# Kernel tuning notes

Hardware: AMD Instinct MI355X
Metric: run time of the kernel (lower is better)

The kernel has to match this reference:

```python
import jax, jax.numpy as jnp
import numpy as np

NUM_LAYERS = 2
SHAPES = [(100, 100), (50, 50), (25, 25), (13, 13)]  # (H, W) per level
D, NH, NP, NL = 256, 8, 4, 4
DH = D // NH
DFF = 1024
B = 2
S = sum(h * w for h, w in SHAPES)  # 13294


def layer_norm(x, g, b, eps=1e-5):
    m = x.mean(-1, keepdims=True)
    v = jnp.var(x, axis=-1, keepdims=True)
    return (x - m) * jax.lax.rsqrt(v + eps) * g + b


def get_reference_points(valid_ratios):
    refs = []
    for lvl, (H_, W_) in enumerate(SHAPES):
        ry, rx = jnp.meshgrid(jnp.linspace(0.5, H_ - 0.5, H_),
                              jnp.linspace(0.5, W_ - 0.5, W_), indexing='ij')
        ry = ry.reshape(-1)[None] / (valid_ratios[:, None, lvl, 1] * H_)
        rx = rx.reshape(-1)[None] / (valid_ratios[:, None, lvl, 0] * W_)
        refs.append(jnp.stack([rx, ry], -1))
    ref = jnp.concatenate(refs, 1)                      # [B, S, 2]
    return ref[:, :, None] * valid_ratios[:, None]      # [B, S, NL, 2]


def sample_level(value_l, H_, W_, loc):
    # value_l: [B, nH, H*W, Dh]; loc: [B, Q, nH, P, 2] normalized in [0,1]
    x = loc[..., 0] * W_ - 0.5
    y = loc[..., 1] * H_ - 0.5
    x0 = jnp.floor(x)
    y0 = jnp.floor(y)
    Bq, Q = loc.shape[0], loc.shape[1]
    acc = 0.
    corners = ((x0, y0, (x0 + 1 - x) * (y0 + 1 - y)),
               (x0 + 1, y0, (x - x0) * (y0 + 1 - y)),
               (x0, y0 + 1, (x0 + 1 - x) * (y - y0)),
               (x0 + 1, y0 + 1, (x - x0) * (y - y0)))
    for xi, yi, w in corners:  # zero-padding grid_sample: invalid corners contribute 0
        valid = (xi >= 0) & (xi <= W_ - 1) & (yi >= 0) & (yi <= H_ - 1)
        idx = (jnp.clip(yi, 0, H_ - 1) * W_ + jnp.clip(xi, 0, W_ - 1)).astype(jnp.int32)
        idx = jnp.transpose(idx, (0, 2, 1, 3)).reshape(Bq, NH, Q * NP)
        g = jnp.take_along_axis(value_l, idx[..., None], axis=2)  # [B,nH,Q*P,Dh]
        wv = jnp.transpose((w * valid).astype(value_l.dtype), (0, 2, 1, 3)).reshape(Bq, NH, Q * NP)
        acc = acc + g * wv[..., None]
    return acc.reshape(Bq, NH, Q, NP, DH)


def msda(query, ref, src, W_val, b_val, W_off, b_off, W_attn, b_attn, W_out, b_out):
    Bq, Q = query.shape[:2]
    value = (src @ W_val + b_val).reshape(Bq, S, NH, DH)
    off = (query @ W_off + b_off).reshape(Bq, Q, NH, NL, NP, 2)
    attn = jax.nn.softmax((query @ W_attn + b_attn).reshape(Bq, Q, NH, NL * NP), -1)
    attn = attn.reshape(Bq, Q, NH, NL, NP)
    normalizer = jnp.array([[w, h] for h, w in SHAPES], dtype=query.dtype)  # [NL,2] (x,y)
    loc = ref[:, :, None, :, None, :] + off / normalizer[None, None, None, :, None, :]
    out = jnp.zeros((Bq, NH, Q, DH), query.dtype)
    start = 0
    for l, (H_, W_) in enumerate(SHAPES):
        v_l = jnp.transpose(value[:, start:start + H_ * W_], (0, 2, 1, 3))  # [B,nH,HW,Dh]
        samp = sample_level(v_l, H_, W_, loc[:, :, :, l])                    # [B,nH,Q,P,Dh]
        w_l = jnp.transpose(attn[:, :, :, l], (0, 2, 1, 3))                  # [B,nH,Q,P]
        out = out + (samp * w_l[..., None]).sum(3)
        start += H_ * W_
    out = jnp.transpose(out, (0, 2, 1, 3)).reshape(Bq, Q, D)
    return out @ W_out + b_out


def setup_inputs() -> dict:
    key = jax.random.key(0)
    ks = jax.random.split(key, 12)
    sc = 0.02
    inp = {
        'src': jax.random.normal(ks[0], (B, S, D), jnp.float32),
        'spatial_shapes': np.array(SHAPES, dtype=np.int64),
        'valid_ratios': jnp.ones((B, NL, 2), jnp.float32),
        'W_off': sc * jax.random.normal(ks[1], (NUM_LAYERS, D, NH * NL * NP * 2), jnp.float32),
        'b_off': jnp.zeros((NUM_LAYERS, NH * NL * NP * 2), jnp.float32),
        'W_attn': sc * jax.random.normal(ks[2], (NUM_LAYERS, D, NH * NL * NP), jnp.float32),
        'b_attn': jnp.zeros((NUM_LAYERS, NH * NL * NP), jnp.float32),
        'W_val': sc * jax.random.normal(ks[3], (NUM_LAYERS, D, D), jnp.float32),
        'b_val': jnp.zeros((NUM_LAYERS, D), jnp.float32),
        'W_out': sc * jax.random.normal(ks[4], (NUM_LAYERS, D, D), jnp.float32),
        'b_out': jnp.zeros((NUM_LAYERS, D), jnp.float32),
        'ln1_g': jnp.ones((NUM_LAYERS, D), jnp.float32),
        'ln1_b': jnp.zeros((NUM_LAYERS, D), jnp.float32),
        'W1': sc * jax.random.normal(ks[5], (NUM_LAYERS, D, DFF), jnp.float32),
        'b1': jnp.zeros((NUM_LAYERS, DFF), jnp.float32),
        'W2': sc * jax.random.normal(ks[6], (NUM_LAYERS, DFF, D), jnp.float32),
        'b2': jnp.zeros((NUM_LAYERS, D), jnp.float32),
        'ln2_g': jnp.ones((NUM_LAYERS, D), jnp.float32),
        'ln2_b': jnp.zeros((NUM_LAYERS, D), jnp.float32),
    }
    return inp


def reference(src, spatial_shapes, valid_ratios, W_off, b_off, W_attn, b_attn,
              W_val, b_val, W_out, b_out, ln1_g, ln1_b, W1, b1, W2, b2, ln2_g, ln2_b):
    # Deformable-DETR encoder stack (dropout=0 / eval mode, pos=None, no padding mask).
    ref = get_reference_points(valid_ratios)  # [B, S, NL, 2]
    x = src
    for i in range(NUM_LAYERS):
        x2 = msda(x, ref, x, W_val[i], b_val[i], W_off[i], b_off[i],
                  W_attn[i], b_attn[i], W_out[i], b_out[i])
        x = layer_norm(x + x2, ln1_g[i], ln1_b[i])
        h = jax.nn.relu(x @ W1[i] + b1[i]) @ W2[i] + b2[i]
        x = layer_norm(x + h, ln2_g[i], ln2_b[i])
    return x
```

## Files before the change

kernel.cpp:

```cpp
#include <hip/hip_runtime.h>
#include <math.h>


#define S_TOT 13294
#define BATCH 2
#define M_TOT (BATCH * S_TOT)
#define M_PAD 26624

typedef __attribute__((ext_vector_type(8))) short short8;
typedef __attribute__((ext_vector_type(4))) float floatx4;

#define AS1C(p) ((const __attribute__((address_space(1))) void*)(p))
#define AS3(p)  ((__attribute__((address_space(3))) void*)(p))

static __device__ __forceinline__ unsigned short f2bf(float x) {
    union { float f; unsigned u; } v; v.f = x;
    unsigned r = v.u + 0x7FFFu + ((v.u >> 16) & 1u);
    return (unsigned short)(r >> 16);
}
static __device__ __forceinline__ float bflo(unsigned u) {
    union { unsigned u; float f; } v; v.u = u << 16; return v.f;
}
static __device__ __forceinline__ float bfhi(unsigned u) {
    union { unsigned u; float f; } v; v.u = u & 0xFFFF0000u; return v.f;
}

template<int TM, bool RELU, bool RES, bool F32OUT, bool BF16OUT, bool PROJ>
__global__ __launch_bounds__(256)
void mgemm(const unsigned short* __restrict__ A,
           const unsigned short* __restrict__ BT,
           const float* __restrict__ bias,
           const float* __restrict__ bias2,
           const float* __restrict__ bias3,
           const float* __restrict__ R,
           float* __restrict__ Cf,
           unsigned short* __restrict__ Cb,
           int M, int N, int K)
{
    constexpr int WM = (TM == 128) ? 2 : 1;
    constexpr int WN = 4 / WM;
    constexpr int MI = TM / (WM * 16);
    constexpr int NI = 128 / (WN * 16);
    __shared__ __align__(16) unsigned short smemA[2 * TM * 32];
    __shared__ __align__(16) unsigned short smemB[2 * 128 * 32];
    const int tid  = threadIdx.x;
    const int lane = tid & 63;
    const int w    = tid >> 6;
    const int wm   = w % WM, wn = w / WM;
    const int lr   = lane & 15, quad = lane >> 4;
    const int bm   = blockIdx.y * TM;
    const int bn   = blockIdx.x * 128;

    floatx4 acc[MI][NI];
    #pragma unroll
    for (int i = 0; i < MI; ++i)
        #pragma unroll
        for (int j = 0; j < NI; ++j)
            acc[i][j] = (floatx4){0.f, 0.f, 0.f, 0.f};

    const int srow = lane >> 2;
    const int selt = (lane & 3) << 3;

    for (int k0 = 0; k0 < K; k0 += 64) {
        #pragma unroll
        for (int c = 0; c < 2; ++c) {
            if (TM == 128) {
                #pragma unroll
                for (int jj = 0; jj < 2; ++jj) {
                    const int j = 2 * w + jj;
                    const unsigned short* ga = A  + (size_t)(bm + j * 16 + srow) * K + k0 + c * 32 + selt;
                    const unsigned short* gb = BT + (size_t)(bn + j * 16 + srow) * K + k0 + c * 32 + selt;
                    __builtin_amdgcn_global_load_lds(AS1C(ga), AS3(smemA + c * (TM * 32) + j * 512), 16, 0, 0);
                    __builtin_amdgcn_global_load_lds(AS1C(gb), AS3(smemB + c * 4096 + j * 512), 16, 0, 0);
                }
            } else {
                const unsigned short* ga = A + (size_t)(bm + w * 16 + srow) * K + k0 + c * 32 + selt;
                __builtin_amdgcn_global_load_lds(AS1C(ga), AS3(smemA + c * (TM * 32) + w * 512), 16, 0, 0);
                #pragma unroll
                for (int jj = 0; jj < 2; ++jj) {
                    const int j = 2 * w + jj;
                    const unsigned short* gb = BT + (size_t)(bn + j * 16 + srow) * K + k0 + c * 32 + selt;
                    __builtin_amdgcn_global_load_lds(AS1C(gb), AS3(smemB + c * 4096 + j * 512), 16, 0, 0);
                }
            }
        }
        __syncthreads();

        #pragma unroll
        for (int c = 0; c < 2; ++c) {
            short8 av[MI], bv[NI];
            #pragma unroll
            for (int mi = 0; mi < MI; ++mi)
                av[mi] = *(const short8*)&smemA[c * (TM * 32) + (wm * MI * 16 + mi * 16 + lr) * 32 + quad * 8];
            #pragma unroll
            for (int ni = 0; ni < NI; ++ni)
                bv[ni] = *(const short8*)&smemB[c * 4096 + (wn * NI * 16 + ni * 16 + lr) * 32 + quad * 8];
            #pragma unroll
            for (int mi = 0; mi < MI; ++mi)
                #pragma unroll
                for (int ni = 0; ni < NI; ++ni)
                    acc[mi][ni] = __builtin_amdgcn_mfma_f32_16x16x32_bf16(
                        av[mi], bv[ni], acc[mi][ni], 0, 0, 0);
        }
        __syncthreads();
    }

    #pragma unroll
    for (int mi = 0; mi < MI; ++mi) {
        #pragma unroll
        for (int ni = 0; ni < NI; ++ni) {
            #pragma unroll
            for (int r = 0; r < 4; ++r) {
                const int row = bm + wm * MI * 16 + mi * 16 + quad * 4 + r;
                const int col = bn + wn * NI * 16 + ni * 16 + lr;
                if (PROJ) {
                    const float bb = (col < 256) ? bias[col]
                                   : (col < 512) ? bias2[col - 256]
                                                 : bias3[col - 512];
                    const float v = acc[mi][ni][r] + bb;
                    if (col < 256) Cb[(size_t)row * 256 + col] = f2bf(v);
                    else           Cf[(size_t)row * 384 + (col - 256)] = v;
                } else {
                    float v = acc[mi][ni][r] + bias[col];
                    if (RES) { if (row < M) v += R[(size_t)row * N + col]; }
                    if (RELU) v = fmaxf(v, 0.0f);
                    if (F32OUT) Cf[(size_t)row * N + col] = v;
                    if (BF16OUT) Cb[(size_t)row * N + col] = f2bf(v);
                }
            }
        }
    }
}

template<bool HASB>
__global__ __launch_bounds__(256)
void mgemm_ln(const unsigned short* __restrict__ A,
              const unsigned short* __restrict__ BT,
              const float* __restrict__ bias,
              const float* __restrict__ R,
              const float* __restrict__ g,
              const float* __restrict__ beta,
              float* __restrict__ outF,
              unsigned short* __restrict__ outB,
              int M, int K)
{
    __shared__ __align__(16) unsigned short smemA[2 * 64 * 32];
    __shared__ __align__(16) unsigned short smemB[2 * 256 * 32];
    const int lane = threadIdx.x & 63;
    const int w    = threadIdx.x >> 6;
    const int lr   = lane & 15, quad = lane >> 4;
    const int bm   = blockIdx.x * 64;
    const int srow = lane >> 2;
    const int selt = (lane & 3) << 3;

    floatx4 acc[4][4];
    #pragma unroll
    for (int i = 0; i < 4; ++i)
        #pragma unroll
        for (int j = 0; j < 4; ++j)
            acc[i][j] = (floatx4){0.f, 0.f, 0.f, 0.f};

    for (int k0 = 0; k0 < K; k0 += 64) {
        #pragma unroll
        for (int c = 0; c < 2; ++c) {
            const unsigned short* ga = A + (size_t)(bm + w * 16 + srow) * K + k0 + c * 32 + selt;
            __builtin_amdgcn_global_load_lds(AS1C(ga), AS3(smemA + c * 2048 + w * 512), 16, 0, 0);
            #pragma unroll
            for (int jj = 0; jj < 4; ++jj) {
                const int j = 4 * w + jj;
                const unsigned short* gb = BT + (size_t)(j * 16 + srow) * K + k0 + c * 32 + selt;
                __builtin_amdgcn_global_load_lds(AS1C(gb), AS3(smemB + c * 8192 + j * 512), 16, 0, 0);
            }
        }
        __syncthreads();
        #pragma unroll
        for (int c = 0; c < 2; ++c) {
            short8 av[4], bv[4];
            #pragma unroll
            for (int mi = 0; mi < 4; ++mi)
                av[mi] = *(const short8*)&smemA[c * 2048 + (mi * 16 + lr) * 32 + quad * 8];
            #pragma unroll
            for (int ni = 0; ni < 4; ++ni)
                bv[ni] = *(const short8*)&smemB[c * 8192 + (w * 64 + ni * 16 + lr) * 32 + quad * 8];
            #pragma unroll
            for (int mi = 0; mi < 4; ++mi)
                #pragma unroll
                for (int ni = 0; ni < 4; ++ni)
                    acc[mi][ni] = __builtin_amdgcn_mfma_f32_16x16x32_bf16(
                        av[mi], bv[ni], acc[mi][ni], 0, 0, 0);
        }
        __syncthreads();
    }

    float bs[4], gs[4], bts[4];
    #pragma unroll
    for (int ni = 0; ni < 4; ++ni) {
        const int col = w * 64 + ni * 16 + lr;
        bs[ni] = bias[col]; gs[ni] = g[col]; bts[ni] = beta[col];
    }
    float* lnbuf = (float*)smemA;

    #pragma unroll
    for (int mi = 0; mi < 4; ++mi) {
        #pragma unroll
        for (int r = 0; r < 4; ++r) {
            const int rl = mi * 16 + quad * 4 + r;
            const int grow = bm + rl;
            const bool act = grow < M;
            float p = 0.f, q = 0.f;
            #pragma unroll
            for (int ni = 0; ni < 4; ++ni) {
                const int col = w * 64 + ni * 16 + lr;
                const float rv = act ? R[(size_t)grow * 256 + col] : 0.f;
                const float x = acc[mi][ni][r] + bs[ni] + rv;
                acc[mi][ni][r] = x;
                p += x; q += x * x;
            }
            #pragma unroll
            for (int o = 1; o < 16; o <<= 1) {
                p += __shfl_xor(p, o, 64);
                q += __shfl_xor(q, o, 64);
            }
            if (lr == 0) {
                lnbuf[rl * 8 + 2 * w]     = p;
                lnbuf[rl * 8 + 2 * w + 1] = q;
            }
        }
    }
    __syncthreads();
    #pragma unroll
    for (int mi = 0; mi < 4; ++mi) {
        #pragma unroll
        for (int r = 0; r < 4; ++r) {
            const int rl = mi * 16 + quad * 4 + r;
            const int grow = bm + rl;
            const float4 pa = *(const float4*)&lnbuf[rl * 8];
            const float4 pb = *(const float4*)&lnbuf[rl * 8 + 4];
            const float s  = pa.x + pa.z + pb.x + pb.z;
            const float s2 = pa.y + pa.w + pb.y + pb.w;
            const float mean = s * (1.0f / 256.0f);
            const float var  = s2 * (1.0f / 256.0f) - mean * mean;
            const float rs   = rsqrtf(var + 1e-5f);
            if (grow < M) {
                #pragma unroll
                for (int ni = 0; ni < 4; ++ni) {
                    const int col = w * 64 + ni * 16 + lr;
                    const float y = (acc[mi][ni][r] - mean) * rs * gs[ni] + bts[ni];
                    outF[(size_t)grow * 256 + col] = y;
                    if (HASB) outB[(size_t)grow * 256 + col] = f2bf(y);
                }
            }
        }
    }
}

__global__ __launch_bounds__(256)
void convpad(const float* __restrict__ X, unsigned short* __restrict__ Y, int M)
{
    const int idx = blockIdx.x * 256 + threadIdx.x;
    const int row = idx >> 6;
    const int c4  = (idx & 63) << 2;
    if (row >= M_PAD) return;
    float4 v = {0.f, 0.f, 0.f, 0.f};
    if (row < M) v = ((const float4*)(X + (size_t)row * 256))[c4 >> 2];
    unsigned p0 = (unsigned)f2bf(v.x) | ((unsigned)f2bf(v.y) << 16);
    unsigned p1 = (unsigned)f2bf(v.z) | ((unsigned)f2bf(v.w) << 16);
    uint2 o; o.x = p0; o.y = p1;
    *(uint2*)(Y + (size_t)row * 256 + c4) = o;
}

struct WJobs {
    const float* W[12];
    unsigned short* WT[12];
    int K[12], N[12], tx[12], start[12];
};

__global__ __launch_bounds__(256)
void wtrans_all(WJobs jb)
{
    __shared__ float t[32][33];
    const int bx = blockIdx.x;
    int seg = 0;
    #pragma unroll
    for (int s = 1; s < 12; ++s) if (bx >= jb.start[s]) seg = s;
    const float* W = jb.W[seg];
    unsigned short* WT = jb.WT[seg];
    const int K = jb.K[seg], N = jb.N[seg], tx = jb.tx[seg];
    const int local = bx - jb.start[seg];
    const int n0 = (local % tx) * 32, k0 = (local / tx) * 32;
    const int c = threadIdx.x & 31, r0 = threadIdx.x >> 5;
    #pragma unroll
    for (int rr = r0; rr < 32; rr += 8)
        t[rr][c] = W[(size_t)(k0 + rr) * N + n0 + c];
    __syncthreads();
    #pragma unroll
    for (int rr = r0; rr < 32; rr += 8)
        WT[(size_t)(n0 + rr) * K + k0 + c] = f2bf(t[c][rr]);
}

__global__ __launch_bounds__(256)
void msda_kernel(const unsigned short* __restrict__ valb,
                 const float* __restrict__ oa,
                 const float* __restrict__ vr,
                 unsigned short* __restrict__ out)
{
    __shared__ __align__(16) char smeta[8 * 128 * 32];
    const int t = threadIdx.x;

    {
        const int wv = t >> 6, lane = t & 63;
        const int lqA = wv * 2 + (lane >> 5);
        const int bq = blockIdx.x * 8 + lqA;
        const int h = (lane >> 2) & 7;
        const int j = lane & 3;
        if (bq < M_TOT) {
            const int b = (bq >= S_TOT) ? 1 : 0;
            const int q = bq - b * S_TOT;
            const int bofs = b * (S_TOT * 512);
            int Hq, rr, cc;
            int lq;
            if (q < 10000)      { lq = 0; Hq = 100; rr = q / 100;              cc = q - rr * 100; }
            else if (q < 12500) { lq = 1; Hq = 50;  int r2 = q - 10000; rr = r2 / 50; cc = r2 - rr * 50; }
            else if (q < 13125) { lq = 2; Hq = 25;  int r2 = q - 12500; rr = r2 / 25; cc = r2 - rr * 25; }
            else                { lq = 3; Hq = 13;  int r2 = q - 13125; rr = r2 / 13; cc = r2 - rr * 13; }
            const float rxb = (cc + 0.5f) / (vr[(b * 4 + lq) * 2 + 0] * (float)Hq);
            const float ryb = (rr + 0.5f) / (vr[(b * 4 + lq) * 2 + 1] * (float)Hq);
            const int HWt[4] = {100, 50, 25, 13};
            const int stt[4] = {0, 10000, 12500, 13125};
            const int HW = HWt[j], st = stt[j];
            const float fW = (float)HW;
            const float refx = rxb * vr[(b * 4 + j) * 2 + 0];
            const float refy = ryb * vr[(b * 4 + j) * 2 + 1];
            const float* row = oa + (size_t)bq * 384;
            const float4 lg = *(const float4*)(row + 256 + h * 16 + j * 4);
            float mx = fmaxf(fmaxf(lg.x, lg.y), fmaxf(lg.z, lg.w));
            mx = fmaxf(mx, __shfl_xor(mx, 1, 64));
            mx = fmaxf(mx, __shfl_xor(mx, 2, 64));
            const float e0 = expf(lg.x - mx), e1 = expf(lg.y - mx);
            const float e2 = expf(lg.z - mx), e3 = expf(lg.w - mx);
            float ss = e0 + e1 + e2 + e3;
            ss += __shfl_xor(ss, 1, 64);
            ss += __shfl_xor(ss, 2, 64);
            const float inv = 1.0f / ss;
            const float4 oA = *(const float4*)(row + h * 32 + j * 8);
            const float4 oB = *(const float4*)(row + h * 32 + j * 8 + 4);
            const float oxs[4] = {oA.x, oA.z, oB.x, oB.z};
            const float oys[4] = {oA.y, oA.w, oB.y, oB.w};
            const float aw[4]  = {e0 * inv, e1 * inv, e2 * inv, e3 * inv};
            char* mb = smeta + (size_t)(lqA * 128 + h * 16 + j * 4) * 32;
            const int swz = ((h * 4 + j) & 7) << 4;
            #pragma unroll
            for (int p = 0; p < 4; ++p) {
                const float x = (refx + oxs[p] / fW) * fW - 0.5f;
                const float y = (refy + oys[p] / fW) * fW - 0.5f;
                const float x0f = floorf(x), y0f = floorf(y);
                const int x0 = (int)x0f, y0 = (int)y0f;
                const float fx = x - x0f, fy = y - y0f;
                const float wb[4] = {(1.f - fx) * (1.f - fy), fx * (1.f - fy),
                                     (1.f - fx) * fy,         fx * fy};
                const int xs[2] = {x0, x0 + 1};
                const int ys2[2] = {y0, y0 + 1};
                int iv[4]; float wv4[4];
                #pragma unroll
                for (int k = 0; k < 4; ++k) {
                    const int xi = xs[k & 1], yi = ys2[k >> 1];
                    const bool vld = ((unsigned)xi < (unsigned)HW) && ((unsigned)yi < (unsigned)HW);
                    const int xc = min(max(xi, 0), HW - 1);
                    const int yc = min(max(yi, 0), HW - 1);
                    iv[k] = bofs + ((st + yc * HW + xc) << 9) + (h << 6);
                    wv4[k] = vld ? wb[k] * aw[p] : 0.0f;
                }
                int4 i4; i4.x = iv[0]; i4.y = iv[1]; i4.z = iv[2]; i4.w = iv[3];
                float4 w4; w4.x = wv4[0]; w4.y = wv4[1]; w4.z = wv4[2]; w4.w = wv4[3];
                *(int4*)(mb + ((p * 32) ^ swz)) = i4;
                *(float4*)(mb + ((p * 32 + 16) ^ swz)) = w4;
            }
        }
    }
    __syncthreads();
    {
        const int lq2 = t >> 5;
        const int r = t & 31;
        const int h2 = r >> 2;
        const int cg = r & 3;
        const int bq2 = blockIdx.x * 8 + lq2;
        if (bq2 < M_TOT) {
            const char* vbase = (const char*)valb;
            const unsigned cgo = cg * 16;
            float acc[8] = {0.f, 0.f, 0.f, 0.f, 0.f, 0.f, 0.f, 0.f};
            const char* mb2 = smeta + (size_t)(lq2 * 128 + h2 * 16) * 32;
            #pragma unroll 4
            for (int s = 0; s < 16; ++s) {
                const int swz2 = ((h2 * 4 + (s >> 2)) & 7) << 4;
                const int4  iv = *(const int4*)(mb2 + ((s * 32) ^ swz2));
                const float4 w4 = *(const float4*)(mb2 + ((s * 32 + 16) ^ swz2));
                const uint4 u0 = *(const uint4*)(vbase + (unsigned)(iv.x + cgo));
                const uint4 u1 = *(const uint4*)(vbase + (unsigned)(iv.y + cgo));
                const uint4 u2 = *(const uint4*)(vbase + (unsigned)(iv.z + cgo));
                const uint4 u3 = *(const uint4*)(vbase + (unsigned)(iv.w + cgo));
                #define ACC8(UU, WW) \
                    acc[0] = fmaf(WW, bflo(UU.x), acc[0]); acc[1] = fmaf(WW, bfhi(UU.x), acc[1]); \
                    acc[2] = fmaf(WW, bflo(UU.y), acc[2]); acc[3] = fmaf(WW, bfhi(UU.y), acc[3]); \
                    acc[4] = fmaf(WW, bflo(UU.z), acc[4]); acc[5] = fmaf(WW, bfhi(UU.z), acc[5]); \
                    acc[6] = fmaf(WW, bflo(UU.w), acc[6]); acc[7] = fmaf(WW, bfhi(UU.w), acc[7]);
                ACC8(u0, w4.x) ACC8(u1, w4.y) ACC8(u2, w4.z) ACC8(u3, w4.w)
                #undef ACC8
            }
            uint4 o;
            o.x = (unsigned)f2bf(acc[0]) | ((unsigned)f2bf(acc[1]) << 16);
            o.y = (unsigned)f2bf(acc[2]) | ((unsigned)f2bf(acc[3]) << 16);
            o.z = (unsigned)f2bf(acc[4]) | ((unsigned)f2bf(acc[5]) << 16);
            o.w = (unsigned)f2bf(acc[6]) | ((unsigned)f2bf(acc[7]) << 16);
            *(uint4*)(out + (size_t)bq2 * 256 + h2 * 32 + cg * 8) = o;
        }
    }
}

extern "C" void kernel_launch(void* const* d_in, const int* in_sizes, int n_in,
                              void* d_out, int out_size, void* d_ws, size_t ws_size,
                              hipStream_t stream)
{
    const float* src    = (const float*)d_in[0];
    const float* vr     = (const float*)d_in[2];
    const float* W_off  = (const float*)d_in[3];
    const float* b_off  = (const float*)d_in[4];
    const float* W_attn = (const float*)d_in[5];
    const float* b_attn = (const float*)d_in[6];
    const float* W_val  = (const float*)d_in[7];
    const float* b_val  = (const float*)d_in[8];
    const float* W_out  = (const float*)d_in[9];
    const float* b_out  = (const float*)d_in[10];
    const float* ln1_g  = (const float*)d_in[11];
    const float* ln1_b  = (const float*)d_in[12];
    const float* W1     = (const float*)d_in[13];
    const float* b1     = (const float*)d_in[14];
    const float* W2     = (const float*)d_in[15];
    const float* b2     = (const float*)d_in[16];
    const float* ln2_g  = (const float*)d_in[17];
    const float* ln2_b  = (const float*)d_in[18];
    float* out = (float*)d_out;

    const int M = M_TOT;

    char* wsb = (char*)d_ws;
    float*          OA   = (float*)wsb;
    unsigned short* VALB = (unsigned short*)(wsb + 40894464);
    unsigned short* HBF  = (unsigned short*)wsb;
    float*          T1   = (float*)(wsb + 54525952);
    unsigned short* RB   = (unsigned short*)(wsb + 81788928);
    unsigned short* YBF  = (unsigned short*)(wsb + 95420416);
    unsigned short* WT   = (unsigned short*)(wsb + 109051904);

    const size_t LWT = 753664;
    const size_t oProj = 0, oOut = 163840, oW1 = 229376, oW2 = 491520;

    WJobs jb;
    int startAcc = 0;
    for (int i = 0; i < 2; ++i) {
        unsigned short* wt = WT + i * LWT;
        const float* srcs[6] = {W_val + i * 65536, W_off + i * 65536, W_attn + i * 32768,
                                W_out + i * 65536, W1 + i * 262144, W2 + i * 262144};
        unsigned short* dsts[6] = {wt + oProj, wt + oProj + 65536, wt + oProj + 131072,
                                   wt + oOut, wt + oW1, wt + oW2};
        const int Ks[6] = {256, 256, 256, 256, 256, 1024};
        const int Ns[6] = {256, 256, 128, 256, 1024, 256};
        for (int s = 0; s < 6; ++s) {
            const int idx = i * 6 + s;
            jb.W[idx] = srcs[s]; jb.WT[idx] = dsts[s];
            jb.K[idx] = Ks[s]; jb.N[idx] = Ns[s]; jb.tx[idx] = Ns[s] / 32;
            jb.start[idx] = startAcc;
            startAcc += (Ns[s] / 32) * (Ks[s] / 32);
        }
    }
    wtrans_all<<<dim3(startAcc), 256, 0, stream>>>(jb);

    const int GM128 = M_PAD / 128;
    const int GM64  = M_PAD / 64;
    const dim3 blk(256);

    for (int i = 0; i < 2; ++i) {
        const float* xin = (i == 0) ? src : out;
        unsigned short* wt = WT + i * LWT;

        if (i == 0)
            convpad<<<dim3(M_PAD / 4), blk, 0, stream>>>(src, RB, M);

        mgemm<64, false, false, false, false, true><<<dim3(5, GM64), blk, 0, stream>>>(
            RB, wt + oProj, b_val + i * 256, b_off + i * 256, b_attn + i * 128,
            nullptr, OA, VALB, M, 640, 256);

        msda_kernel<<<dim3((M + 7) / 8), blk, 0, stream>>>(VALB, OA, vr, YBF);

        mgemm_ln<true><<<dim3(GM64), blk, 0, stream>>>(
            YBF, wt + oOut, b_out + i * 256, xin,
            ln1_g + i * 256, ln1_b + i * 256, T1, RB, M, 256);

        mgemm<128, true, false, false, true, false><<<dim3(8, GM128), blk, 0, stream>>>(
            RB, wt + oW1, b1 + i * 1024, nullptr, nullptr,
            nullptr, nullptr, HBF, M, 1024, 256);

        if (i == 0)
            mgemm_ln<true><<<dim3(GM64), blk, 0, stream>>>(
                HBF, wt + oW2, b2 + i * 256, T1,
                ln2_g + i * 256, ln2_b + i * 256, out, RB, M, 1024);
        else
            mgemm_ln<false><<<dim3(GM64), blk, 0, stream>>>(
                HBF, wt + oW2, b2 + i * 256, T1,
                ln2_g + i * 256, ln2_b + i * 256, out, nullptr, M, 1024);
    }
}
```

Measured before the change: 456.6 us.

## Store offsets/logits in bf16, shrink LN-GEMM tile, pack MSDA accumulation

The projection GEMM now writes the sampling offsets and attention logits as bf16 instead of fp32, so the MSDA kernel reads half the bytes. MSDA also folds the reference scaling into a precomputed term, uses fast exp, and accumulates in packed float2 vectors. The fused GEMM+LayerNorm kernel drops its row tile from 64 to 32, doubling the block count for better occupancy across CUs. These changes reduce precision of the offsets and logits, which can shift sampling positions, and the smaller tile reloads the weight matrix from memory more often.

```diff
diff --git a/kernel.cpp b/kernel.cpp
--- a/kernel.cpp
+++ b/kernel.cpp
@@ -9,6 +9,7 @@
 
 typedef __attribute__((ext_vector_type(8))) short short8;
 typedef __attribute__((ext_vector_type(4))) float floatx4;
+typedef __attribute__((ext_vector_type(2))) float floatx2;
 
 #define AS1C(p) ((const __attribute__((address_space(1))) void*)(p))
 #define AS3(p)  ((__attribute__((address_space(3))) void*)(p))
@@ -35,6 +36,7 @@
            const float* __restrict__ R,
            float* __restrict__ Cf,
            unsigned short* __restrict__ Cb,
+           unsigned short* __restrict__ Cb2,
            int M, int N, int K)
 {
     constexpr int WM = (TM == 128) ? 2 : 1;
@@ -119,7 +121,7 @@
                                                  : bias3[col - 512];
                     const float v = acc[mi][ni][r] + bb;
                     if (col < 256) Cb[(size_t)row * 256 + col] = f2bf(v);
-                    else           Cf[(size_t)row * 384 + (col - 256)] = v;
+                    else           Cb2[(size_t)row * 384 + (col - 256)] = f2bf(v);
                 } else {
                     float v = acc[mi][ni][r] + bias[col];
                     if (RES) { if (row < M) v += R[(size_t)row * N + col]; }
@@ -144,27 +146,28 @@
               unsigned short* __restrict__ outB,
               int M, int K)
 {
-    __shared__ __align__(16) unsigned short smemA[2 * 64 * 32];
+    __shared__ __align__(16) unsigned short smemA[2 * 32 * 32];
     __shared__ __align__(16) unsigned short smemB[2 * 256 * 32];
     const int lane = threadIdx.x & 63;
     const int w    = threadIdx.x >> 6;
     const int lr   = lane & 15, quad = lane >> 4;
-    const int bm   = blockIdx.x * 64;
+    const int bm   = blockIdx.x * 32;
     const int srow = lane >> 2;
     const int selt = (lane & 3) << 3;
-
-    floatx4 acc[4][4];
-    #pragma unroll
-    for (int i = 0; i < 4; ++i)
+    const int cA = w >> 1, rh = w & 1;
+
+    floatx4 acc[2][4];
+    #pragma unroll
+    for (int i = 0; i < 2; ++i)
         #pragma unroll
         for (int j = 0; j < 4; ++j)
             acc[i][j] = (floatx4){0.f, 0.f, 0.f, 0.f};
 
     for (int k0 = 0; k0 < K; k0 += 64) {
+        const unsigned short* ga = A + (size_t)(bm + rh * 16 + srow) * K + k0 + cA * 32 + selt;
+        __builtin_amdgcn_global_load_lds(AS1C(ga), AS3(smemA + cA * 1024 + rh * 512), 16, 0, 0);
         #pragma unroll
         for (int c = 0; c < 2; ++c) {
-            const unsigned short* ga = A + (size_t)(bm + w * 16 + srow) * K + k0 + c * 32 + selt;
-            __builtin_amdgcn_global_load_lds(AS1C(ga), AS3(smemA + c * 2048 + w * 512), 16, 0, 0);
             #pragma unroll
             for (int jj = 0; jj < 4; ++jj) {
                 const int j = 4 * w + jj;
@@ -175,15 +178,15 @@
         __syncthreads();
         #pragma unroll
         for (int c = 0; c < 2; ++c) {
-            short8 av[4], bv[4];
-            #pragma unroll
-            for (int mi = 0; mi < 4; ++mi)
-                av[mi] = *(const short8*)&smemA[c * 2048 + (mi * 16 + lr) * 32 + quad * 8];
+            short8 av[2], bv[4];
+            #pragma unroll
+            for (int mi = 0; mi < 2; ++mi)
+                av[mi] = *(const short8*)&smemA[c * 1024 + (mi * 16 + lr) * 32 + quad * 8];
             #pragma unroll
             for (int ni = 0; ni < 4; ++ni)
                 bv[ni] = *(const short8*)&smemB[c * 8192 + (w * 64 + ni * 16 + lr) * 32 + quad * 8];
             #pragma unroll
-            for (int mi = 0; mi < 4; ++mi)
+            for (int mi = 0; mi < 2; ++mi)
                 #pragma unroll
                 for (int ni = 0; ni < 4; ++ni)
                     acc[mi][ni] = __builtin_amdgcn_mfma_f32_16x16x32_bf16(
@@ -201,7 +204,7 @@
     float* lnbuf = (float*)smemA;
 
     #pragma unroll
-    for (int mi = 0; mi < 4; ++mi) {
+    for (int mi = 0; mi < 2; ++mi) {
         #pragma unroll
         for (int r = 0; r < 4; ++r) {
             const int rl = mi * 16 + quad * 4 + r;
@@ -229,7 +232,7 @@
     }
     __syncthreads();
     #pragma unroll
-    for (int mi = 0; mi < 4; ++mi) {
+    for (int mi = 0; mi < 2; ++mi) {
         #pragma unroll
         for (int r = 0; r < 4; ++r) {
             const int rl = mi * 16 + quad * 4 + r;
@@ -300,7 +303,7 @@
 
 __global__ __launch_bounds__(256)
 void msda_kernel(const unsigned short* __restrict__ valb,
-                 const float* __restrict__ oa,
+                 const unsigned short* __restrict__ oab,
                  const float* __restrict__ vr,
                  unsigned short* __restrict__ out)
 {
@@ -317,8 +320,7 @@
             const int b = (bq >= S_TOT) ? 1 : 0;
             const int q = bq - b * S_TOT;
             const int bofs = b * (S_TOT * 512);
-            int Hq, rr, cc;
-            int lq;
+            int Hq, rr, cc, lq;
             if (q < 10000)      { lq = 0; Hq = 100; rr = q / 100;              cc = q - rr * 100; }
             else if (q < 12500) { lq = 1; Hq = 50;  int r2 = q - 10000; rr = r2 / 50; cc = r2 - rr * 50; }
             else if (q < 13125) { lq = 2; Hq = 25;  int r2 = q - 12500; rr = r2 / 25; cc = r2 - rr * 25; }
@@ -329,30 +331,31 @@
             const int stt[4] = {0, 10000, 12500, 13125};
             const int HW = HWt[j], st = stt[j];
             const float fW = (float)HW;
-            const float refx = rxb * vr[(b * 4 + j) * 2 + 0];
-            const float refy = ryb * vr[(b * 4 + j) * 2 + 1];
-            const float* row = oa + (size_t)bq * 384;
-            const float4 lg = *(const float4*)(row + 256 + h * 16 + j * 4);
-            float mx = fmaxf(fmaxf(lg.x, lg.y), fmaxf(lg.z, lg.w));
+            const float refxw = rxb * vr[(b * 4 + j) * 2 + 0] * fW - 0.5f;
+            const float refyw = ryb * vr[(b * 4 + j) * 2 + 1] * fW - 0.5f;
+            const unsigned short* row = oab + (size_t)bq * 384;
+            const uint2 lgu = *(const uint2*)(row + 256 + h * 16 + j * 4);
+            const float l0 = bflo(lgu.x), l1 = bfhi(lgu.x);
+            const float l2 = bflo(lgu.y), l3 = bfhi(lgu.y);
+            float mx = fmaxf(fmaxf(l0, l1), fmaxf(l2, l3));
             mx = fmaxf(mx, __shfl_xor(mx, 1, 64));
             mx = fmaxf(mx, __shfl_xor(mx, 2, 64));
-            const float e0 = expf(lg.x - mx), e1 = expf(lg.y - mx);
-            const float e2 = expf(lg.z - mx), e3 = expf(lg.w - mx);
+            const float e0 = __expf(l0 - mx), e1 = __expf(l1 - mx);
+            const float e2 = __expf(l2 - mx), e3 = __expf(l3 - mx);
             float ss = e0 + e1 + e2 + e3;
             ss += __shfl_xor(ss, 1, 64);
             ss += __shfl_xor(ss, 2, 64);
             const float inv = 1.0f / ss;
-            const float4 oA = *(const float4*)(row + h * 32 + j * 8);
-            const float4 oB = *(const float4*)(row + h * 32 + j * 8 + 4);
-            const float oxs[4] = {oA.x, oA.z, oB.x, oB.z};
-            const float oys[4] = {oA.y, oA.w, oB.y, oB.w};
+            const uint4 ou = *(const uint4*)(row + h * 32 + j * 8);
+            const float oxs[4] = {bflo(ou.x), bflo(ou.y), bflo(ou.z), bflo(ou.w)};
+            const float oys[4] = {bfhi(ou.x), bfhi(ou.y), bfhi(ou.z), bfhi(ou.w)};
             const float aw[4]  = {e0 * inv, e1 * inv, e2 * inv, e3 * inv};
             char* mb = smeta + (size_t)(lqA * 128 + h * 16 + j * 4) * 32;
             const int swz = ((h * 4 + j) & 7) << 4;
             #pragma unroll
             for (int p = 0; p < 4; ++p) {
-                const float x = (refx + oxs[p] / fW) * fW - 0.5f;
-                const float y = (refy + oys[p] / fW) * fW - 0.5f;
+                const float x = refxw + oxs[p];
+                const float y = refyw + oys[p];
                 const float x0f = floorf(x), y0f = floorf(y);
                 const int x0 = (int)x0f, y0 = (int)y0f;
                 const float fx = x - x0f, fy = y - y0f;
@@ -387,7 +390,7 @@
         if (bq2 < M_TOT) {
             const char* vbase = (const char*)valb;
             const unsigned cgo = cg * 16;
-            float acc[8] = {0.f, 0.f, 0.f, 0.f, 0.f, 0.f, 0.f, 0.f};
+            floatx2 a0 = {0.f, 0.f}, a1 = {0.f, 0.f}, a2 = {0.f, 0.f}, a3 = {0.f, 0.f};
             const char* mb2 = smeta + (size_t)(lq2 * 128 + h2 * 16) * 32;
             #pragma unroll 4
             for (int s = 0; s < 16; ++s) {
@@ -398,19 +401,21 @@
                 const uint4 u1 = *(const uint4*)(vbase + (unsigned)(iv.y + cgo));
                 const uint4 u2 = *(const uint4*)(vbase + (unsigned)(iv.z + cgo));
                 const uint4 u3 = *(const uint4*)(vbase + (unsigned)(iv.w + cgo));
-                #define ACC8(UU, WW) \
-                    acc[0] = fmaf(WW, bflo(UU.x), acc[0]); acc[1] = fmaf(WW, bfhi(UU.x), acc[1]); \
-                    acc[2] = fmaf(WW, bflo(UU.y), acc[2]); acc[3] = fmaf(WW, bfhi(UU.y), acc[3]); \
-                    acc[4] = fmaf(WW, bflo(UU.z), acc[4]); acc[5] = fmaf(WW, bfhi(UU.z), acc[5]); \
-                    acc[6] = fmaf(WW, bflo(UU.w), acc[6]); acc[7] = fmaf(WW, bfhi(UU.w), acc[7]);
+                #define ACC8(UU, WW) { \
+                    const floatx2 w2 = {WW, WW}; \
+                    const floatx2 t0 = {bflo(UU.x), bfhi(UU.x)}; \
+                    const floatx2 t1 = {bflo(UU.y), bfhi(UU.y)}; \
+                    const floatx2 t2 = {bflo(UU.z), bfhi(UU.z)}; \
+                    const floatx2 t3 = {bflo(UU.w), bfhi(UU.w)}; \
+                    a0 += w2 * t0; a1 += w2 * t1; a2 += w2 * t2; a3 += w2 * t3; }
                 ACC8(u0, w4.x) ACC8(u1, w4.y) ACC8(u2, w4.z) ACC8(u3, w4.w)
                 #undef ACC8
             }
             uint4 o;
-            o.x = (unsigned)f2bf(acc[0]) | ((unsigned)f2bf(acc[1]) << 16);
-            o.y = (unsigned)f2bf(acc[2]) | ((unsigned)f2bf(acc[3]) << 16);
-            o.z = (unsigned)f2bf(acc[4]) | ((unsigned)f2bf(acc[5]) << 16);
-            o.w = (unsigned)f2bf(acc[6]) | ((unsigned)f2bf(acc[7]) << 16);
+            o.x = (unsigned)f2bf(a0.x) | ((unsigned)f2bf(a0.y) << 16);
+            o.y = (unsigned)f2bf(a1.x) | ((unsigned)f2bf(a1.y) << 16);
+            o.z = (unsigned)f2bf(a2.x) | ((unsigned)f2bf(a2.y) << 16);
+            o.w = (unsigned)f2bf(a3.x) | ((unsigned)f2bf(a3.y) << 16);
             *(uint4*)(out + (size_t)bq2 * 256 + h2 * 32 + cg * 8) = o;
         }
     }
@@ -443,9 +448,9 @@
     const int M = M_TOT;
 
     char* wsb = (char*)d_ws;
-    float*          OA   = (float*)wsb;
-    unsigned short* VALB = (unsigned short*)(wsb + 40894464);
     unsigned short* HBF  = (unsigned short*)wsb;
+    unsigned short* OAB  = (unsigned short*)wsb;
+    unsigned short* VALB = (unsigned short*)(wsb + 20447232);
     float*          T1   = (float*)(wsb + 54525952);
     unsigned short* RB   = (unsigned short*)(wsb + 81788928);
     unsigned short* YBF  = (unsigned short*)(wsb + 95420416);
@@ -476,6 +481,7 @@
 
     const int GM128 = M_PAD / 128;
     const int GM64  = M_PAD / 64;
+    const int GL32  = M_PAD / 32;
     const dim3 blk(256);
 
     for (int i = 0; i < 2; ++i) {
@@ -487,24 +493,24 @@
 
         mgemm<64, false, false, false, false, true><<<dim3(5, GM64), blk, 0, stream>>>(
             RB, wt + oProj, b_val + i * 256, b_off + i * 256, b_attn + i * 128,
-            nullptr, OA, VALB, M, 640, 256);
-
-        msda_kernel<<<dim3((M + 7) / 8), blk, 0, stream>>>(VALB, OA, vr, YBF);
-
-        mgemm_ln<true><<<dim3(GM64), blk, 0, stream>>>(
+            nullptr, nullptr, VALB, OAB, M, 640, 256);
+
+        msda_kernel<<<dim3((M + 7) / 8), blk, 0, stream>>>(VALB, OAB, vr, YBF);
+
+        mgemm_ln<true><<<dim3(GL32), blk, 0, stream>>>(
             YBF, wt + oOut, b_out + i * 256, xin,
             ln1_g + i * 256, ln1_b + i * 256, T1, RB, M, 256);
 
         mgemm<128, true, false, false, true, false><<<dim3(8, GM128), blk, 0, stream>>>(
             RB, wt + oW1, b1 + i * 1024, nullptr, nullptr,
-            nullptr, nullptr, HBF, M, 1024, 256);
+            nullptr, nullptr, HBF, nullptr, M, 1024, 256);
 
         if (i == 0)
-            mgemm_ln<true><<<dim3(GM64), blk, 0, stream>>>(
+            mgemm_ln<true><<<dim3(GL32), blk, 0, stream>>>(
                 HBF, wt + oW2, b2 + i * 256, T1,
                 ln2_g + i * 256, ln2_b + i * 256, out, RB, M, 1024);
         else
-            mgemm_ln<false><<<dim3(GM64), blk, 0, stream>>>(
+            mgemm_ln<false><<<dim3(GL32), blk, 0, stream>>>(
                 HBF, wt + oW2, b2 + i * 256, T1,
                 ln2_g + i * 256, ln2_b + i * 256, out, nullptr, M, 1024);
     }
```

Measured after the change: 455.5 us. About the same (-0.2%).
